# Kernel tuning notes

Hardware: AMD Instinct MI355X
Metric: run time of the kernel (lower is better)

The kernel has to match this reference:

```python
import jax, jax.numpy as jnp
import numpy as np
import math

HIDDEN = 256
D = 256  # attention_head_size (num_heads=1)
LN_EPS = 1e-5


def setup_inputs() -> dict:
    key = jax.random.key(0)
    ks = jax.random.split(key, 12)
    b, n = 8, 256
    s = 0.02
    return {
        "hidden_states": jax.random.normal(ks[0], (b, n, HIDDEN), jnp.float32),
        "structure_matrix": jax.random.normal(ks[1], (b, n, n, D), jnp.float32),
        "Wq": jax.random.normal(ks[2], (HIDDEN, D), jnp.float32) * s,
        "bq": jnp.zeros((D,), jnp.float32),
        "Wk": jax.random.normal(ks[3], (D, D), jnp.float32) * s,
        "bk": jnp.zeros((D,), jnp.float32),
        "Wv": jax.random.normal(ks[4], (HIDDEN, D), jnp.float32) * s,
        "bv": jnp.zeros((D,), jnp.float32),
        "Wo": jax.random.normal(ks[5], (D, D), jnp.float32) * s,
        "bo": jnp.zeros((D,), jnp.float32),
        "ln_gamma": jnp.ones((D,), jnp.float32),
        "ln_beta": jnp.zeros((D,), jnp.float32),
    }


def _layer_norm(x, gamma, beta):
    mu = jnp.mean(x, axis=-1, keepdims=True)
    var = jnp.mean(jnp.square(x - mu), axis=-1, keepdims=True)
    return (x - mu) * jax.lax.rsqrt(var + LN_EPS) * gamma + beta


def reference(hidden_states, structure_matrix, Wq, bq, Wk, bk, Wv, bv, Wo, bo, ln_gamma, ln_beta):
    # projections
    q = hidden_states @ Wq + bq            # [b, n, d]
    k = structure_matrix @ Wk + bk         # [b, l, r, d]
    v = hidden_states @ Wv + bv            # [b, n, d]
    # pair-biased attention: each (l, r) pair attends over all n tokens
    scores = jnp.einsum('bnd,blrd->blrn', q, k) / math.sqrt(D)  # [b, l, r, n]
    probs = jax.nn.softmax(scores, axis=-1)  # dropout is identity in eval
    ctx = jnp.einsum('blrn,bnd->blrd', probs, v)  # [b, l, r, d]
    out = ctx @ Wo + bo
    return _layer_norm(out + structure_matrix, ln_gamma, ln_beta)
```

## Files before the change

### kernel.cpp

```cpp
#include <hip/hip_runtime.h>
#include <hip/hip_bf16.h>

typedef __attribute__((ext_vector_type(8))) short short8v;
typedef __attribute__((ext_vector_type(4))) float f32x4;
typedef __attribute__((ext_vector_type(4))) unsigned short us4;
typedef __attribute__((ext_vector_type(8))) unsigned short us8;

#define LDA 264

__device__ __forceinline__ unsigned short f2bf(float f) {
  union { __hip_bfloat16 h; unsigned short u; } c;
  c.h = __float2bfloat16(f);
  return c.u;
}
__device__ __forceinline__ unsigned int f2bf2(float lo, float hi) {
  union { __hip_bfloat162 h; unsigned int u; } c;
  c.h = __float22bfloat162_rn(make_float2(lo, hi));
  return c.u;
}

__global__ __launch_bounds__(256) void make_w(
    const float* __restrict__ Wq, const float* __restrict__ Wk,
    const float* __restrict__ Wv, const float* __restrict__ Wo,
    const float* __restrict__ bq, const float* __restrict__ bk,
    const float* __restrict__ bv, float* __restrict__ WA,
    float* __restrict__ WB, float* __restrict__ wb2,
    float* __restrict__ cq, float* __restrict__ cv, float* __restrict__ cb) {
  __shared__ float wq[256], wv[256], bqs[256], bvs[256];
  const int i = blockIdx.x, t = threadIdx.x;
  wq[t] = Wq[i * 256 + t];
  wv[t] = Wv[i * 256 + t];
  bqs[t] = bq[t];
  bvs[t] = bv[t];
  __syncthreads();
  float sa = 0.f, sb = 0.f;
  for (int d = 0; d < 256; d++) {
    sa = fmaf(wq[d], Wk[t * 256 + d], sa);
    sb = fmaf(wv[d], Wo[d * 256 + t], sb);
  }
  WA[i * 256 + t] = sa * 0.0625f;
  WB[i * 256 + t] = sb;
  if (t == 0) {
    float s = 0.f;
    for (int d = 0; d < 256; d++) s = fmaf(wq[d], bk[d], s);
    wb2[i] = s * 0.0625f;
  }
  if (i == 0) {
    float s1 = 0.f, s2 = 0.f;
    for (int d = 0; d < 256; d++) {
      s1 = fmaf(bqs[d], Wk[t * 256 + d], s1);
      s2 = fmaf(bvs[d], Wo[d * 256 + t], s2);
    }
    cq[t] = s1 * 0.0625f;
    cv[t] = s2;
    if (t == 0) {
      float s = 0.f;
      for (int d = 0; d < 256; d++) s = fmaf(bk[d], bqs[d], s);
      cb[0] = s * 0.0625f;
    }
  }
}

__global__ __launch_bounds__(256) void prep2(
    const float* __restrict__ hs, const float* __restrict__ WA,
    const float* __restrict__ WB, const float* __restrict__ wb2,
    const float* __restrict__ cq, const float* __restrict__ cv,
    const float* __restrict__ cb, unsigned short* __restrict__ W2B,
    unsigned short* __restrict__ V2B, float* __restrict__ bn) {
  __shared__ float rows[8][256];
  __shared__ float w2s[256];
  const int tid = threadIdx.x;
  const int g0 = blockIdx.x * 8;
#pragma unroll
  for (int j = 0; j < 8; j++) rows[j][tid] = hs[(size_t)(g0 + j) * 256 + tid];
  w2s[tid] = wb2[tid];
  __syncthreads();
  const float cqv = cq[tid], cvv = cv[tid];
  float aq[8], av[8];
#pragma unroll
  for (int j = 0; j < 8; j++) { aq[j] = cqv; av[j] = cvv; }
  for (int i = 0; i < 256; i++) {
    const float wa = WA[i * 256 + tid];
    const float wb = WB[i * 256 + tid];
#pragma unroll
    for (int j = 0; j < 8; j++) {
      aq[j] = fmaf(rows[j][i], wa, aq[j]);
      av[j] = fmaf(rows[j][i], wb, av[j]);
    }
  }
  const int bb = g0 >> 8, n0 = g0 & 255;
#pragma unroll
  for (int j = 0; j < 8; j++)
    W2B[(size_t)(bb * 256 + n0 + j) * 256 + tid] = f2bf(aq[j]);
  us8 vp;
#pragma unroll
  for (int j = 0; j < 8; j++) vp[j] = f2bf(av[j]);
  *(us8*)(V2B + (size_t)(bb * 256 + tid) * 256 + n0) = vp;
  if (tid < 8) {
    float s = 0.f;
    for (int i = 0; i < 256; i++) s = fmaf(rows[tid][i], w2s[i], s);
    bn[bb * 256 + n0 + tid] = s + cb[0];
  }
}

__device__ __forceinline__ void mm64x256(
    const unsigned short* sAp, const unsigned short* __restrict__ Bg,
    int w, int l16, int lhi, f32x4 acc[4][4]) {
#pragma unroll
  for (int rt = 0; rt < 4; rt++)
#pragma unroll
    for (int nt = 0; nt < 4; nt++) acc[rt][nt] = (f32x4){0.f, 0.f, 0.f, 0.f};
#pragma unroll 2
  for (int k0 = 0; k0 < 256; k0 += 32) {
    const int kk = k0 + lhi * 8;
    short8v a[4], bfr[4];
#pragma unroll
    for (int rt = 0; rt < 4; rt++)
      a[rt] = *(const short8v*)(sAp + (rt * 16 + l16) * LDA + kk);
#pragma unroll
    for (int nt = 0; nt < 4; nt++)
      bfr[nt] = *(const short8v*)(Bg + (w * 64 + nt * 16 + l16) * 256 + kk);
#pragma unroll
    for (int rt = 0; rt < 4; rt++)
#pragma unroll
      for (int nt = 0; nt < 4; nt++)
        acc[rt][nt] = __builtin_amdgcn_mfma_f32_16x16x32_bf16(
            a[rt], bfr[nt], acc[rt][nt], 0, 0, 0);
  }
}

__device__ __forceinline__ void mm64x256_ps(
    const unsigned short* sAp, const unsigned short* __restrict__ Bg,
    int w, int l16, int lhi, f32x4 acc[4][4], f32x4 ps[4]) {
  short8v onesv;
#pragma unroll
  for (int j = 0; j < 8; j++) onesv[j] = (short)0x3F80;
#pragma unroll
  for (int rt = 0; rt < 4; rt++) {
    ps[rt] = (f32x4){0.f, 0.f, 0.f, 0.f};
#pragma unroll
    for (int nt = 0; nt < 4; nt++) acc[rt][nt] = (f32x4){0.f, 0.f, 0.f, 0.f};
  }
#pragma unroll 2
  for (int k0 = 0; k0 < 256; k0 += 32) {
    const int kk = k0 + lhi * 8;
    short8v a[4], bfr[4];
#pragma unroll
    for (int rt = 0; rt < 4; rt++)
      a[rt] = *(const short8v*)(sAp + (rt * 16 + l16) * LDA + kk);
#pragma unroll
    for (int nt = 0; nt < 4; nt++)
      bfr[nt] = *(const short8v*)(Bg + (w * 64 + nt * 16 + l16) * 256 + kk);
#pragma unroll
    for (int rt = 0; rt < 4; rt++) {
#pragma unroll
      for (int nt = 0; nt < 4; nt++)
        acc[rt][nt] = __builtin_amdgcn_mfma_f32_16x16x32_bf16(
            a[rt], bfr[nt], acc[rt][nt], 0, 0, 0);
      ps[rt] = __builtin_amdgcn_mfma_f32_16x16x32_bf16(a[rt], onesv, ps[rt],
                                                       0, 0, 0);
    }
  }
}

__global__ __launch_bounds__(256, 4) void pair_attn2(
    const float* __restrict__ S, const float* __restrict__ bo,
    const float* __restrict__ gamma, const float* __restrict__ beta,
    const float* __restrict__ bn, const unsigned short* __restrict__ W2B,
    const unsigned short* __restrict__ V2B, float* __restrict__ out) {
  __shared__ unsigned short sA[64 * LDA];
  __shared__ float sRed[64 * 8];

  const int tid = threadIdx.x;
  const int w = tid >> 6;
  const int lane = tid & 63;
  const int l16 = lane & 15;
  const int lhi = lane >> 4;
  const int bid = blockIdx.x;
  const int idx = (bid & 7) * 1024 + (bid >> 3);
  const int rblk = idx & 3;
  const int lrow = (idx >> 2) & 255;
  const int bat = idx >> 10;

  const size_t base = ((size_t)((bat * 256 + lrow) * 256 + rblk * 64)) * 256;
  const float* Sblk = S + base;

#pragma unroll
  for (int it = 0; it < 8; it++) {
    const int c = tid + it * 256;
    const int row = c >> 5, col = (c & 31) << 3;
    const float4 u = *(const float4*)(Sblk + row * 256 + col);
    const float4 v = *(const float4*)(Sblk + row * 256 + col + 4);
    us8 p;
    unsigned int* pu = (unsigned int*)&p;
    pu[0] = f2bf2(u.x, u.y);
    pu[1] = f2bf2(u.z, u.w);
    pu[2] = f2bf2(v.x, v.y);
    pu[3] = f2bf2(v.z, v.w);
    *(us8*)(sA + row * LDA + col) = p;
  }
  float bnv[4];
#pragma unroll
  for (int nt = 0; nt < 4; nt++)
    bnv[nt] = bn[bat * 256 + w * 64 + nt * 16 + l16];
  __syncthreads();

  f32x4 acc[4][4];

  mm64x256(sA, W2B + (size_t)bat * 65536, w, l16, lhi, acc);
  __syncthreads();

#pragma unroll
  for (int rt = 0; rt < 4; rt++)
#pragma unroll
    for (int nt = 0; nt < 4; nt++)
#pragma unroll
      for (int rg = 0; rg < 4; rg++)
        sA[(rt * 16 + lhi * 4 + rg) * LDA + (w * 64 + nt * 16 + l16)] =
            f2bf(__expf(acc[rt][nt][rg] + bnv[nt]));
  __syncthreads();

  f32x4 ps[4];
  mm64x256_ps(sA, V2B + (size_t)bat * 65536, w, l16, lhi, acc, ps);

  float bov[4], gv[4], bev[4];
#pragma unroll
  for (int nt = 0; nt < 4; nt++) {
    const int col = w * 64 + nt * 16 + l16;
    bov[nt] = bo[col];
    gv[nt] = gamma[col];
    bev[nt] = beta[col];
  }
#pragma unroll
  for (int rt = 0; rt < 4; rt++)
#pragma unroll
    for (int rg = 0; rg < 4; rg++) {
      const int row = rt * 16 + lhi * 4 + rg;
      const float invr = 1.f / ps[rt][rg];
      float s1 = 0.f, s2 = 0.f;
#pragma unroll
      for (int nt = 0; nt < 4; nt++) {
        const int col = w * 64 + nt * 16 + l16;
        const float val =
            acc[rt][nt][rg] * invr + bov[nt] + Sblk[row * 256 + col];
        acc[rt][nt][rg] = val;
        s1 += val;
        s2 = fmaf(val, val, s2);
      }
      s1 += __shfl_xor(s1, 1); s2 += __shfl_xor(s2, 1);
      s1 += __shfl_xor(s1, 2); s2 += __shfl_xor(s2, 2);
      s1 += __shfl_xor(s1, 4); s2 += __shfl_xor(s2, 4);
      s1 += __shfl_xor(s1, 8); s2 += __shfl_xor(s2, 8);
      if (l16 == 0) { sRed[row * 8 + w] = s1; sRed[row * 8 + 4 + w] = s2; }
    }
  __syncthreads();

  float* O = out + base;
#pragma unroll
  for (int rt = 0; rt < 4; rt++)
#pragma unroll
    for (int rg = 0; rg < 4; rg++) {
      const int row = rt * 16 + lhi * 4 + rg;
      f32x4 sa = *(f32x4*)(sRed + row * 8);
      f32x4 sq = *(f32x4*)(sRed + row * 8 + 4);
      const float mean = (sa[0] + sa[1] + sa[2] + sa[3]) * (1.f / 256.f);
      const float ex2 = (sq[0] + sq[1] + sq[2] + sq[3]) * (1.f / 256.f);
      const float rstd = rsqrtf(ex2 - mean * mean + 1e-5f);
#pragma unroll
      for (int nt = 0; nt < 4; nt++) {
        const int col = w * 64 + nt * 16 + l16;
        O[row * 256 + col] = (acc[rt][nt][rg] - mean) * rstd * gv[nt] + bev[nt];
      }
    }
}

extern "C" void kernel_launch(void* const* d_in, const int* in_sizes, int n_in,
                              void* d_out, int out_size, void* d_ws, size_t ws_size,
                              hipStream_t stream) {
  const float* hs    = (const float*)d_in[0];
  const float* S     = (const float*)d_in[1];
  const float* Wq    = (const float*)d_in[2];
  const float* bq    = (const float*)d_in[3];
  const float* Wk    = (const float*)d_in[4];
  const float* bk    = (const float*)d_in[5];
  const float* Wv    = (const float*)d_in[6];
  const float* bv    = (const float*)d_in[7];
  const float* Wo    = (const float*)d_in[8];
  const float* bo    = (const float*)d_in[9];
  const float* gamma = (const float*)d_in[10];
  const float* beta  = (const float*)d_in[11];

  unsigned short* W2B = (unsigned short*)d_ws;
  unsigned short* V2B = W2B + 8 * 256 * 256;
  float* WA  = (float*)(V2B + 8 * 256 * 256);
  float* WB  = WA + 256 * 256;
  float* wb2 = WB + 256 * 256;
  float* cq  = wb2 + 256;
  float* cv  = cq + 256;
  float* cb  = cv + 256;
  float* bnp = cb + 256;

  make_w<<<256, 256, 0, stream>>>(Wq, Wk, Wv, Wo, bq, bk, bv, WA, WB, wb2, cq,
                                  cv, cb);
  prep2<<<256, 256, 0, stream>>>(hs, WA, WB, wb2, cq, cv, cb, W2B, V2B, bnp);
  pair_attn2<<<8192, 256, 0, stream>>>(S, bo, gamma, beta, bnp, W2B, V2B,
                                       (float*)d_out);
}
```

Baseline: 556.5 us.

## Make pair attention blocks loop over four tiles with register prefetch of next tile

The main kernel now launches a quarter as many blocks, and each block handles four consecutive 64-row tiles of the same batch. While the current tile's matmuls and epilogue run, the block loads the next tile of the structure matrix into registers, converts it to bf16, and writes it to shared memory at the end of the iteration. The aim is to hide global load latency and amortise per-block setup such as the bias and gamma loads. The 16 float4 prefetch registers raise register pressure under launch_bounds(256,4), which may cause spills or lower occupancy. The batch-interleaved block ordering is also changed.

```diff
diff --git a/kernel.cpp b/kernel.cpp
--- a/kernel.cpp
+++ b/kernel.cpp
@@ -7,6 +7,7 @@
 typedef __attribute__((ext_vector_type(8))) unsigned short us8;
 
 #define LDA 264
+#define ITERS 4
 
 __device__ __forceinline__ unsigned short f2bf(float f) {
   union { __hip_bfloat16 h; unsigned short u; } c;
@@ -163,7 +164,7 @@
   }
 }
 
-__global__ __launch_bounds__(256, 4) void pair_attn2(
+__global__ __launch_bounds__(256, 4) void pair_attn3(
     const float* __restrict__ S, const float* __restrict__ bo,
     const float* __restrict__ gamma, const float* __restrict__ beta,
     const float* __restrict__ bn, const unsigned short* __restrict__ W2B,
@@ -177,101 +178,147 @@
   const int l16 = lane & 15;
   const int lhi = lane >> 4;
   const int bid = blockIdx.x;
-  const int idx = (bid & 7) * 1024 + (bid >> 3);
-  const int rblk = idx & 3;
-  const int lrow = (idx >> 2) & 255;
-  const int bat = idx >> 10;
-
-  const size_t base = ((size_t)((bat * 256 + lrow) * 256 + rblk * 64)) * 256;
-  const float* Sblk = S + base;
-
-#pragma unroll
-  for (int it = 0; it < 8; it++) {
-    const int c = tid + it * 256;
-    const int row = c >> 5, col = (c & 31) << 3;
-    const float4 u = *(const float4*)(Sblk + row * 256 + col);
-    const float4 v = *(const float4*)(Sblk + row * 256 + col + 4);
-    us8 p;
-    unsigned int* pu = (unsigned int*)&p;
-    pu[0] = f2bf2(u.x, u.y);
-    pu[1] = f2bf2(u.z, u.w);
-    pu[2] = f2bf2(v.x, v.y);
-    pu[3] = f2bf2(v.z, v.w);
-    *(us8*)(sA + row * LDA + col) = p;
-  }
-  float bnv[4];
-#pragma unroll
-  for (int nt = 0; nt < 4; nt++)
-    bnv[nt] = bn[bat * 256 + w * 64 + nt * 16 + l16];
-  __syncthreads();
-
-  f32x4 acc[4][4];
-
-  mm64x256(sA, W2B + (size_t)bat * 65536, w, l16, lhi, acc);
-  __syncthreads();
-
-#pragma unroll
-  for (int rt = 0; rt < 4; rt++)
-#pragma unroll
-    for (int nt = 0; nt < 4; nt++)
-#pragma unroll
-      for (int rg = 0; rg < 4; rg++)
-        sA[(rt * 16 + lhi * 4 + rg) * LDA + (w * 64 + nt * 16 + l16)] =
-            f2bf(__expf(acc[rt][nt][rg] + bnv[nt]));
-  __syncthreads();
-
-  f32x4 ps[4];
-  mm64x256_ps(sA, V2B + (size_t)bat * 65536, w, l16, lhi, acc, ps);
-
-  float bov[4], gv[4], bev[4];
+  const int bat = bid & 7;
+  const int local = bid >> 3;
+
+  const unsigned short* W2b = W2B + (size_t)bat * 65536;
+  const unsigned short* V2b = V2B + (size_t)bat * 65536;
+
+  float bnv[4], bov[4], gv[4], bev[4];
 #pragma unroll
   for (int nt = 0; nt < 4; nt++) {
     const int col = w * 64 + nt * 16 + l16;
+    bnv[nt] = bn[bat * 256 + col];
     bov[nt] = bo[col];
     gv[nt] = gamma[col];
     bev[nt] = beta[col];
   }
-#pragma unroll
-  for (int rt = 0; rt < 4; rt++)
-#pragma unroll
-    for (int rg = 0; rg < 4; rg++) {
-      const int row = rt * 16 + lhi * 4 + rg;
-      const float invr = 1.f / ps[rt][rg];
-      float s1 = 0.f, s2 = 0.f;
-#pragma unroll
-      for (int nt = 0; nt < 4; nt++) {
-        const int col = w * 64 + nt * 16 + l16;
-        const float val =
-            acc[rt][nt][rg] * invr + bov[nt] + Sblk[row * 256 + col];
-        acc[rt][nt][rg] = val;
-        s1 += val;
-        s2 = fmaf(val, val, s2);
-      }
-      s1 += __shfl_xor(s1, 1); s2 += __shfl_xor(s2, 1);
-      s1 += __shfl_xor(s1, 2); s2 += __shfl_xor(s2, 2);
-      s1 += __shfl_xor(s1, 4); s2 += __shfl_xor(s2, 4);
-      s1 += __shfl_xor(s1, 8); s2 += __shfl_xor(s2, 8);
-      if (l16 == 0) { sRed[row * 8 + w] = s1; sRed[row * 8 + 4 + w] = s2; }
-    }
+
+  {
+    const int t0 = local * ITERS;
+    const float* Sb =
+        S + ((size_t)((bat * 256 + (t0 >> 2)) * 256 + (t0 & 3) * 64)) * 256;
+#pragma unroll
+    for (int j = 0; j < 8; j++) {
+      const int c = tid + j * 256;
+      const int row = c >> 5, col = (c & 31) << 3;
+      const float4 u = *(const float4*)(Sb + row * 256 + col);
+      const float4 v = *(const float4*)(Sb + row * 256 + col + 4);
+      us8 p;
+      unsigned int* pu = (unsigned int*)&p;
+      pu[0] = f2bf2(u.x, u.y);
+      pu[1] = f2bf2(u.z, u.w);
+      pu[2] = f2bf2(v.x, v.y);
+      pu[3] = f2bf2(v.z, v.w);
+      *(us8*)(sA + row * LDA + col) = p;
+    }
+  }
   __syncthreads();
 
-  float* O = out + base;
-#pragma unroll
-  for (int rt = 0; rt < 4; rt++)
-#pragma unroll
-    for (int rg = 0; rg < 4; rg++) {
-      const int row = rt * 16 + lhi * 4 + rg;
-      f32x4 sa = *(f32x4*)(sRed + row * 8);
-      f32x4 sq = *(f32x4*)(sRed + row * 8 + 4);
-      const float mean = (sa[0] + sa[1] + sa[2] + sa[3]) * (1.f / 256.f);
-      const float ex2 = (sq[0] + sq[1] + sq[2] + sq[3]) * (1.f / 256.f);
-      const float rstd = rsqrtf(ex2 - mean * mean + 1e-5f);
-#pragma unroll
-      for (int nt = 0; nt < 4; nt++) {
-        const int col = w * 64 + nt * 16 + l16;
-        O[row * 256 + col] = (acc[rt][nt][rg] - mean) * rstd * gv[nt] + bev[nt];
-      }
-    }
+  for (int it = 0; it < ITERS; ++it) {
+    const int tileid = local * ITERS + it;
+    const size_t base =
+        ((size_t)((bat * 256 + (tileid >> 2)) * 256 + (tileid & 3) * 64)) * 256;
+    const float* Sblk = S + base;
+    const bool havenext = (it + 1 < ITERS);
+
+    f32x4 acc[4][4];
+
+    mm64x256(sA, W2b, w, l16, lhi, acc);
+
+    float4 pf[16];
+    if (havenext) {
+      const int t2 = tileid + 1;
+      const float* Sn =
+          S + ((size_t)((bat * 256 + (t2 >> 2)) * 256 + (t2 & 3) * 64)) * 256;
+#pragma unroll
+      for (int j = 0; j < 8; j++) {
+        const int c = tid + j * 256;
+        const int row = c >> 5, col = (c & 31) << 3;
+        pf[2 * j] = *(const float4*)(Sn + row * 256 + col);
+        pf[2 * j + 1] = *(const float4*)(Sn + row * 256 + col + 4);
+      }
+    }
+    __syncthreads();
+
+#pragma unroll
+    for (int rt = 0; rt < 4; rt++)
+#pragma unroll
+      for (int nt = 0; nt < 4; nt++)
+#pragma unroll
+        for (int rg = 0; rg < 4; rg++)
+          sA[(rt * 16 + lhi * 4 + rg) * LDA + (w * 64 + nt * 16 + l16)] =
+              f2bf(__expf(acc[rt][nt][rg] + bnv[nt]));
+    __syncthreads();
+
+    f32x4 ps[4];
+    mm64x256_ps(sA, V2b, w, l16, lhi, acc, ps);
+
+    us8 pb[8];
+    if (havenext) {
+#pragma unroll
+      for (int j = 0; j < 8; j++) {
+        unsigned int* pu = (unsigned int*)&pb[j];
+        pu[0] = f2bf2(pf[2 * j].x, pf[2 * j].y);
+        pu[1] = f2bf2(pf[2 * j].z, pf[2 * j].w);
+        pu[2] = f2bf2(pf[2 * j + 1].x, pf[2 * j + 1].y);
+        pu[3] = f2bf2(pf[2 * j + 1].z, pf[2 * j + 1].w);
+      }
+    }
+
+#pragma unroll
+    for (int rt = 0; rt < 4; rt++)
+#pragma unroll
+      for (int rg = 0; rg < 4; rg++) {
+        const int row = rt * 16 + lhi * 4 + rg;
+        const float invr = 1.f / ps[rt][rg];
+        float s1 = 0.f, s2 = 0.f;
+#pragma unroll
+        for (int nt = 0; nt < 4; nt++) {
+          const int col = w * 64 + nt * 16 + l16;
+          const float val =
+              acc[rt][nt][rg] * invr + bov[nt] + Sblk[row * 256 + col];
+          acc[rt][nt][rg] = val;
+          s1 += val;
+          s2 = fmaf(val, val, s2);
+        }
+        s1 += __shfl_xor(s1, 1); s2 += __shfl_xor(s2, 1);
+        s1 += __shfl_xor(s1, 2); s2 += __shfl_xor(s2, 2);
+        s1 += __shfl_xor(s1, 4); s2 += __shfl_xor(s2, 4);
+        s1 += __shfl_xor(s1, 8); s2 += __shfl_xor(s2, 8);
+        if (l16 == 0) { sRed[row * 8 + w] = s1; sRed[row * 8 + 4 + w] = s2; }
+      }
+    __syncthreads();
+
+    float* O = out + base;
+#pragma unroll
+    for (int rt = 0; rt < 4; rt++)
+#pragma unroll
+      for (int rg = 0; rg < 4; rg++) {
+        const int row = rt * 16 + lhi * 4 + rg;
+        f32x4 sa = *(f32x4*)(sRed + row * 8);
+        f32x4 sq = *(f32x4*)(sRed + row * 8 + 4);
+        const float mean = (sa[0] + sa[1] + sa[2] + sa[3]) * (1.f / 256.f);
+        const float ex2 = (sq[0] + sq[1] + sq[2] + sq[3]) * (1.f / 256.f);
+        const float rstd = rsqrtf(ex2 - mean * mean + 1e-5f);
+#pragma unroll
+        for (int nt = 0; nt < 4; nt++) {
+          const int col = w * 64 + nt * 16 + l16;
+          O[row * 256 + col] =
+              (acc[rt][nt][rg] - mean) * rstd * gv[nt] + bev[nt];
+        }
+      }
+
+    if (havenext) {
+#pragma unroll
+      for (int j = 0; j < 8; j++) {
+        const int c = tid + j * 256;
+        const int row = c >> 5, col = (c & 31) << 3;
+        *(us8*)(sA + row * LDA + col) = pb[j];
+      }
+    }
+    __syncthreads();
+  }
 }
 
 extern "C" void kernel_launch(void* const* d_in, const int* in_sizes, int n_in,
@@ -303,6 +350,6 @@
   make_w<<<256, 256, 0, stream>>>(Wq, Wk, Wv, Wo, bq, bk, bv, WA, WB, wb2, cq,
                                   cv, cb);
   prep2<<<256, 256, 0, stream>>>(hs, WA, WB, wb2, cq, cv, cb, W2B, V2B, bnp);
-  pair_attn2<<<8192, 256, 0, stream>>>(S, bo, gamma, beta, bnp, W2B, V2B,
+  pair_attn3<<<2048, 256, 0, stream>>>(S, bo, gamma, beta, bnp, W2B, V2B,
                                        (float*)d_out);
 }
```

New measurement: 1.584 ms. 185% more time.

## Stage B operands into LDS via async global_load_lds double buffering

Applied to the files above, without the earlier changes.

Reorders W2/V2 weight matrices into 32-wide K-chunk blocks and streams them into a double-buffered LDS region with global_load_lds, overlapping the next chunk's load with the current chunk's MFMA work across both GEMMs. Previously every wave read its B fragments straight from global memory inside the MFMA loop. The extra 32 KB of LDS drops occupancy to 2 blocks per CU, and manual waitcnt/barrier handling adds ordering risk. The small prep kernels also gain unroll pragmas.

```diff
diff --git a/kernel.cpp b/kernel.cpp
--- a/kernel.cpp
+++ b/kernel.cpp
@@ -3,8 +3,9 @@
 
 typedef __attribute__((ext_vector_type(8))) short short8v;
 typedef __attribute__((ext_vector_type(4))) float f32x4;
-typedef __attribute__((ext_vector_type(4))) unsigned short us4;
 typedef __attribute__((ext_vector_type(8))) unsigned short us8;
+typedef const __attribute__((address_space(1))) void* gas_t;
+typedef __attribute__((address_space(3))) void* las_t;
 
 #define LDA 264
 
@@ -34,6 +35,7 @@
   bvs[t] = bv[t];
   __syncthreads();
   float sa = 0.f, sb = 0.f;
+#pragma unroll 8
   for (int d = 0; d < 256; d++) {
     sa = fmaf(wq[d], Wk[t * 256 + d], sa);
     sb = fmaf(wv[d], Wo[d * 256 + t], sb);
@@ -42,11 +44,13 @@
   WB[i * 256 + t] = sb;
   if (t == 0) {
     float s = 0.f;
+#pragma unroll 8
     for (int d = 0; d < 256; d++) s = fmaf(wq[d], bk[d], s);
     wb2[i] = s * 0.0625f;
   }
   if (i == 0) {
     float s1 = 0.f, s2 = 0.f;
+#pragma unroll 8
     for (int d = 0; d < 256; d++) {
       s1 = fmaf(bqs[d], Wk[t * 256 + d], s1);
       s2 = fmaf(bvs[d], Wo[d * 256 + t], s2);
@@ -65,8 +69,8 @@
     const float* __restrict__ hs, const float* __restrict__ WA,
     const float* __restrict__ WB, const float* __restrict__ wb2,
     const float* __restrict__ cq, const float* __restrict__ cv,
-    const float* __restrict__ cb, unsigned short* __restrict__ W2B,
-    unsigned short* __restrict__ V2B, float* __restrict__ bn) {
+    const float* __restrict__ cb, unsigned short* __restrict__ W2c,
+    unsigned short* __restrict__ V2c, float* __restrict__ bn) {
   __shared__ float rows[8][256];
   __shared__ float w2s[256];
   const int tid = threadIdx.x;
@@ -79,6 +83,7 @@
   float aq[8], av[8];
 #pragma unroll
   for (int j = 0; j < 8; j++) { aq[j] = cqv; av[j] = cvv; }
+#pragma unroll 8
   for (int i = 0; i < 256; i++) {
     const float wa = WA[i * 256 + tid];
     const float wb = WB[i * 256 + tid];
@@ -91,11 +96,12 @@
   const int bb = g0 >> 8, n0 = g0 & 255;
 #pragma unroll
   for (int j = 0; j < 8; j++)
-    W2B[(size_t)(bb * 256 + n0 + j) * 256 + tid] = f2bf(aq[j]);
+    W2c[bb * 65536 + (tid >> 5) * 8192 + (n0 + j) * 32 + (tid & 31)] =
+        f2bf(aq[j]);
   us8 vp;
 #pragma unroll
   for (int j = 0; j < 8; j++) vp[j] = f2bf(av[j]);
-  *(us8*)(V2B + (size_t)(bb * 256 + tid) * 256 + n0) = vp;
+  *(us8*)(V2c + bb * 65536 + (n0 >> 5) * 8192 + tid * 32 + (n0 & 31)) = vp;
   if (tid < 8) {
     float s = 0.f;
     for (int i = 0; i < 256; i++) s = fmaf(rows[tid][i], w2s[i], s);
@@ -103,72 +109,23 @@
   }
 }
 
-__device__ __forceinline__ void mm64x256(
-    const unsigned short* sAp, const unsigned short* __restrict__ Bg,
-    int w, int l16, int lhi, f32x4 acc[4][4]) {
-#pragma unroll
-  for (int rt = 0; rt < 4; rt++)
-#pragma unroll
-    for (int nt = 0; nt < 4; nt++) acc[rt][nt] = (f32x4){0.f, 0.f, 0.f, 0.f};
-#pragma unroll 2
-  for (int k0 = 0; k0 < 256; k0 += 32) {
-    const int kk = k0 + lhi * 8;
-    short8v a[4], bfr[4];
-#pragma unroll
-    for (int rt = 0; rt < 4; rt++)
-      a[rt] = *(const short8v*)(sAp + (rt * 16 + l16) * LDA + kk);
-#pragma unroll
-    for (int nt = 0; nt < 4; nt++)
-      bfr[nt] = *(const short8v*)(Bg + (w * 64 + nt * 16 + l16) * 256 + kk);
-#pragma unroll
-    for (int rt = 0; rt < 4; rt++)
-#pragma unroll
-      for (int nt = 0; nt < 4; nt++)
-        acc[rt][nt] = __builtin_amdgcn_mfma_f32_16x16x32_bf16(
-            a[rt], bfr[nt], acc[rt][nt], 0, 0, 0);
-  }
-}
-
-__device__ __forceinline__ void mm64x256_ps(
-    const unsigned short* sAp, const unsigned short* __restrict__ Bg,
-    int w, int l16, int lhi, f32x4 acc[4][4], f32x4 ps[4]) {
-  short8v onesv;
-#pragma unroll
-  for (int j = 0; j < 8; j++) onesv[j] = (short)0x3F80;
-#pragma unroll
-  for (int rt = 0; rt < 4; rt++) {
-    ps[rt] = (f32x4){0.f, 0.f, 0.f, 0.f};
-#pragma unroll
-    for (int nt = 0; nt < 4; nt++) acc[rt][nt] = (f32x4){0.f, 0.f, 0.f, 0.f};
-  }
-#pragma unroll 2
-  for (int k0 = 0; k0 < 256; k0 += 32) {
-    const int kk = k0 + lhi * 8;
-    short8v a[4], bfr[4];
-#pragma unroll
-    for (int rt = 0; rt < 4; rt++)
-      a[rt] = *(const short8v*)(sAp + (rt * 16 + l16) * LDA + kk);
-#pragma unroll
-    for (int nt = 0; nt < 4; nt++)
-      bfr[nt] = *(const short8v*)(Bg + (w * 64 + nt * 16 + l16) * 256 + kk);
-#pragma unroll
-    for (int rt = 0; rt < 4; rt++) {
-#pragma unroll
-      for (int nt = 0; nt < 4; nt++)
-        acc[rt][nt] = __builtin_amdgcn_mfma_f32_16x16x32_bf16(
-            a[rt], bfr[nt], acc[rt][nt], 0, 0, 0);
-      ps[rt] = __builtin_amdgcn_mfma_f32_16x16x32_bf16(a[rt], onesv, ps[rt],
-                                                       0, 0, 0);
-    }
-  }
-}
-
-__global__ __launch_bounds__(256, 4) void pair_attn2(
+__device__ __forceinline__ void stage_b(const unsigned short* src_wave,
+                                        unsigned short* lds_wave, int lane) {
+#pragma unroll
+  for (int i = 0; i < 4; i++) {
+    const unsigned short* g = src_wave + i * 512 + lane * 8;
+    unsigned short* l = lds_wave + i * 512;
+    __builtin_amdgcn_global_load_lds((gas_t)g, (las_t)l, 16, 0, 0);
+  }
+}
+
+__global__ __launch_bounds__(256, 2) void pair_attn9(
     const float* __restrict__ S, const float* __restrict__ bo,
     const float* __restrict__ gamma, const float* __restrict__ beta,
-    const float* __restrict__ bn, const unsigned short* __restrict__ W2B,
-    const unsigned short* __restrict__ V2B, float* __restrict__ out) {
+    const float* __restrict__ bn, const unsigned short* __restrict__ W2c,
+    const unsigned short* __restrict__ V2c, float* __restrict__ out) {
   __shared__ unsigned short sA[64 * LDA];
+  __shared__ unsigned short sB[2][8192];
   __shared__ float sRed[64 * 8];
 
   const int tid = threadIdx.x;
@@ -205,11 +162,49 @@
     bnv[nt] = bn[bat * 256 + w * 64 + nt * 16 + l16];
   __syncthreads();
 
+  const unsigned short* W2b = W2c + (size_t)bat * 65536;
+  const unsigned short* V2b = V2c + (size_t)bat * 65536;
+
+  asm volatile("s_waitcnt vmcnt(0)" ::: "memory");
+  __builtin_amdgcn_sched_barrier(0);
+
+  stage_b(W2b + 0 * 8192 + w * 2048, &sB[0][w * 2048], lane);
+  stage_b(W2b + 1 * 8192 + w * 2048, &sB[1][w * 2048], lane);
+
   f32x4 acc[4][4];
-
-  mm64x256(sA, W2B + (size_t)bat * 65536, w, l16, lhi, acc);
-  __syncthreads();
-
+#pragma unroll
+  for (int rt = 0; rt < 4; rt++)
+#pragma unroll
+    for (int nt = 0; nt < 4; nt++) acc[rt][nt] = (f32x4){0.f, 0.f, 0.f, 0.f};
+
+#pragma unroll
+  for (int q = 0; q < 8; q++) {
+    asm volatile("s_waitcnt vmcnt(4)" ::: "memory");
+    __builtin_amdgcn_sched_barrier(0);
+    const unsigned short* bb = &sB[q & 1][w * 2048];
+    short8v a[4], bf[4];
+#pragma unroll
+    for (int rt = 0; rt < 4; rt++)
+      a[rt] = *(const short8v*)(sA + (rt * 16 + l16) * LDA + q * 32 + lhi * 8);
+#pragma unroll
+    for (int nt = 0; nt < 4; nt++)
+      bf[nt] = *(const short8v*)(bb + (nt * 16 + l16) * 32 + lhi * 8);
+#pragma unroll
+    for (int rt = 0; rt < 4; rt++)
+#pragma unroll
+      for (int nt = 0; nt < 4; nt++)
+        acc[rt][nt] = __builtin_amdgcn_mfma_f32_16x16x32_bf16(
+            a[rt], bf[nt], acc[rt][nt], 0, 0, 0);
+    asm volatile("s_waitcnt lgkmcnt(0)" ::: "memory");
+    __builtin_amdgcn_sched_barrier(0);
+    if (q < 6)
+      stage_b(W2b + (q + 2) * 8192 + w * 2048, &sB[q & 1][w * 2048], lane);
+    else
+      stage_b(V2b + (q - 6) * 8192 + w * 2048, &sB[q & 1][w * 2048], lane);
+  }
+
+  asm volatile("s_waitcnt lgkmcnt(0)" ::: "memory");
+  __builtin_amdgcn_s_barrier();
 #pragma unroll
   for (int rt = 0; rt < 4; rt++)
 #pragma unroll
@@ -218,10 +213,50 @@
       for (int rg = 0; rg < 4; rg++)
         sA[(rt * 16 + lhi * 4 + rg) * LDA + (w * 64 + nt * 16 + l16)] =
             f2bf(__expf(acc[rt][nt][rg] + bnv[nt]));
-  __syncthreads();
-
+  asm volatile("s_waitcnt lgkmcnt(0)" ::: "memory");
+  __builtin_amdgcn_s_barrier();
+
+  short8v onesv;
+#pragma unroll
+  for (int j = 0; j < 8; j++) onesv[j] = (short)0x3F80;
   f32x4 ps[4];
-  mm64x256_ps(sA, V2B + (size_t)bat * 65536, w, l16, lhi, acc, ps);
+#pragma unroll
+  for (int rt = 0; rt < 4; rt++) {
+    ps[rt] = (f32x4){0.f, 0.f, 0.f, 0.f};
+#pragma unroll
+    for (int nt = 0; nt < 4; nt++) acc[rt][nt] = (f32x4){0.f, 0.f, 0.f, 0.f};
+  }
+#pragma unroll
+  for (int q = 0; q < 8; q++) {
+    if (q < 7) {
+      asm volatile("s_waitcnt vmcnt(4)" ::: "memory");
+    } else {
+      asm volatile("s_waitcnt vmcnt(0)" ::: "memory");
+    }
+    __builtin_amdgcn_sched_barrier(0);
+    const unsigned short* bb = &sB[q & 1][w * 2048];
+    short8v a[4], bf[4];
+#pragma unroll
+    for (int rt = 0; rt < 4; rt++)
+      a[rt] = *(const short8v*)(sA + (rt * 16 + l16) * LDA + q * 32 + lhi * 8);
+#pragma unroll
+    for (int nt = 0; nt < 4; nt++)
+      bf[nt] = *(const short8v*)(bb + (nt * 16 + l16) * 32 + lhi * 8);
+#pragma unroll
+    for (int rt = 0; rt < 4; rt++) {
+#pragma unroll
+      for (int nt = 0; nt < 4; nt++)
+        acc[rt][nt] = __builtin_amdgcn_mfma_f32_16x16x32_bf16(
+            a[rt], bf[nt], acc[rt][nt], 0, 0, 0);
+      ps[rt] = __builtin_amdgcn_mfma_f32_16x16x32_bf16(a[rt], onesv, ps[rt],
+                                                       0, 0, 0);
+    }
+    asm volatile("s_waitcnt lgkmcnt(0)" ::: "memory");
+    __builtin_amdgcn_sched_barrier(0);
+    if (q < 6)
+      stage_b(V2b + (q + 2) * 8192 + w * 2048, &sB[q & 1][w * 2048], lane);
+  }
+  __builtin_amdgcn_sched_barrier(0);
 
   float bov[4], gv[4], bev[4];
 #pragma unroll
@@ -237,12 +272,12 @@
     for (int rg = 0; rg < 4; rg++) {
       const int row = rt * 16 + lhi * 4 + rg;
       const float invr = 1.f / ps[rt][rg];
+      const float* Srow = Sblk + row * 256;
       float s1 = 0.f, s2 = 0.f;
 #pragma unroll
       for (int nt = 0; nt < 4; nt++) {
         const int col = w * 64 + nt * 16 + l16;
-        const float val =
-            acc[rt][nt][rg] * invr + bov[nt] + Sblk[row * 256 + col];
+        const float val = acc[rt][nt][rg] * invr + bov[nt] + Srow[col];
         acc[rt][nt][rg] = val;
         s1 += val;
         s2 = fmaf(val, val, s2);
@@ -266,10 +301,11 @@
       const float mean = (sa[0] + sa[1] + sa[2] + sa[3]) * (1.f / 256.f);
       const float ex2 = (sq[0] + sq[1] + sq[2] + sq[3]) * (1.f / 256.f);
       const float rstd = rsqrtf(ex2 - mean * mean + 1e-5f);
+      float* Orow = O + row * 256;
 #pragma unroll
       for (int nt = 0; nt < 4; nt++) {
         const int col = w * 64 + nt * 16 + l16;
-        O[row * 256 + col] = (acc[rt][nt][rg] - mean) * rstd * gv[nt] + bev[nt];
+        Orow[col] = (acc[rt][nt][rg] - mean) * rstd * gv[nt] + bev[nt];
       }
     }
 }
@@ -290,9 +326,9 @@
   const float* gamma = (const float*)d_in[10];
   const float* beta  = (const float*)d_in[11];
 
-  unsigned short* W2B = (unsigned short*)d_ws;
-  unsigned short* V2B = W2B + 8 * 256 * 256;
-  float* WA  = (float*)(V2B + 8 * 256 * 256);
+  unsigned short* W2c = (unsigned short*)d_ws;
+  unsigned short* V2c = W2c + 8 * 256 * 256;
+  float* WA  = (float*)(V2c + 8 * 256 * 256);
   float* WB  = WA + 256 * 256;
   float* wb2 = WB + 256 * 256;
   float* cq  = wb2 + 256;
@@ -302,7 +338,7 @@
 
   make_w<<<256, 256, 0, stream>>>(Wq, Wk, Wv, Wo, bq, bk, bv, WA, WB, wb2, cq,
                                   cv, cb);
-  prep2<<<256, 256, 0, stream>>>(hs, WA, WB, wb2, cq, cv, cb, W2B, V2B, bnp);
-  pair_attn2<<<8192, 256, 0, stream>>>(S, bo, gamma, beta, bnp, W2B, V2B,
+  prep2<<<256, 256, 0, stream>>>(hs, WA, WB, wb2, cq, cv, cb, W2c, V2c, bnp);
+  pair_attn9<<<8192, 256, 0, stream>>>(S, bo, gamma, beta, bnp, W2c, V2c,
                                        (float*)d_out);
 }
```

Result: faster. 524.5 us (-5.8%).
